# Kernel tuning notes

Hardware: AMD Instinct MI355X
Metric: run time of the kernel (lower is better)

Reference implementation:

```python
import jax, jax.numpy as jnp
import numpy as np

N_Q = 8
DIM = 2 ** N_Q          # 256
DEGREE = 3
ANSATZ_LAYERS = 2


def gelu(x):
    return jax.nn.gelu(x, approximate=False)


def layer_norm(x, g, b, eps=1e-5):
    mu = x.mean(-1, keepdims=True)
    v = x.var(-1, keepdims=True)
    return (x - mu) / jnp.sqrt(v + eps) * g + b


def apply_ry(state, theta, w, n):
    # state: (B, 2^n) complex64, theta: (B,) per-element angle
    half = theta * 0.5
    c, s = jnp.cos(half), jnp.sin(half)
    U = jnp.stack([jnp.stack([c, -s], -1), jnp.stack([s, c], -1)], -2).astype(state.dtype)
    L, R = 2 ** w, 2 ** (n - 1 - w)
    st = state.reshape(-1, L, 2, R)
    st = jnp.einsum('bij,bljr->blir', U, st)
    return st.reshape(state.shape)


def apply_crx(state, theta, c, t, n):
    # controlled-RX(theta), control wire c, target wire t (batched angles)
    half = theta * 0.5
    cs = jnp.cos(half).astype(state.dtype)
    ms = (-1j) * jnp.sin(half).astype(state.dtype)
    Rx = jnp.stack([jnp.stack([cs, ms], -1), jnp.stack([ms, cs], -1)], -2)  # (B,2,2)
    a, b = min(c, t), max(c, t)
    A, M, R = 2 ** a, 2 ** (b - a - 1), 2 ** (n - 1 - b)
    st = state.reshape(-1, A, 2, M, 2, R)
    if c < t:
        sub = st[:, :, 1]                              # control bit = 1 slice, (B,A,M,2,R)
        sub = jnp.einsum('bij,bamjr->bamir', Rx, sub)
        st = st.at[:, :, 1].set(sub)
    else:
        sub = st[:, :, :, :, 1]                        # (B,A,2,M,R)
        sub = jnp.einsum('bij,bajmr->baimr', Rx, sub)
        st = st.at[:, :, :, :, 1].set(sub)
    return st.reshape(state.shape)


def sim14(state, params, n, layers):
    # Sim et al. 2019 circuit 14: RY layer, CRX ring, RY layer, reversed CRX ring (4n params/layer)
    idx = 0
    for _ in range(layers):
        for q in range(n):
            state = apply_ry(state, params[:, idx + q], q, n)
        idx += n
        for q in range(n):
            state = apply_crx(state, params[:, idx + q], q, (q + 1) % n, n)
        idx += n
        for q in range(n):
            state = apply_ry(state, params[:, idx + q], q, n)
        idx += n
        for q in range(n):
            state = apply_crx(state, params[:, idx + q], q, (q - 1) % n, n)
        idx += n
    return state


def pauli_expvals(psi, n):
    # [<X_0..X_{n-1}>, <Y_0..>, <Z_0..>] for batched pure states psi: (B, 2^n)
    xs, ys, zs = [], [], []
    for w in range(n):
        L, R = 2 ** w, 2 ** (n - 1 - w)
        s = psi.reshape(-1, L, 2, R)
        s0, s1 = s[:, :, 0], s[:, :, 1]
        cross = (jnp.conj(s0) * s1).sum((1, 2))
        xs.append(2.0 * jnp.real(cross))
        ys.append(2.0 * jnp.imag(cross))
        zs.append((jnp.abs(s0) ** 2 - jnp.abs(s1) ** 2).sum((1, 2)))
    return jnp.stack(xs + ys + zs, axis=1).astype(jnp.float32)


def dwsep_conv(x, dw_w, dw_b, pw_w, pw_b, gn_g, gn_b, dilation):
    # depthwise-separable conv1d + GroupNorm(8) + GELU; x: (B, C, T)
    k = dw_w.shape[-1]
    pad = (k - 1) * dilation // 2
    y = jax.lax.conv_general_dilated(
        x, dw_w, window_strides=(1,), padding=[(pad, pad)], rhs_dilation=(dilation,),
        feature_group_count=x.shape[1], dimension_numbers=('NCH', 'OIH', 'NCH'))
    y = y + dw_b[None, :, None]
    y = jnp.einsum('oc,bct->bot', pw_w, y) + pw_b[None, :, None]
    B, C, T = y.shape
    g = y.reshape(B, 8, C // 8, T)
    mu = g.mean((2, 3), keepdims=True)
    var = g.var((2, 3), keepdims=True)
    y = ((g - mu) / jnp.sqrt(var + 1e-5)).reshape(B, C, T)
    return gelu(y * gn_g[None, :, None] + gn_b[None, :, None])


def setup_inputs() -> dict:
    key = jax.random.key(0)
    ks = iter(jax.random.split(key, 64))
    rn = lambda *s: jax.random.normal(next(ks), s, jnp.float32) * 0.05
    ru = lambda *s: jax.random.uniform(next(ks), s, dtype=jnp.float32)
    inp = dict(
        x=jax.random.normal(next(ks), (16, 363, 180), jnp.float32),
        net_w=rn(12, 15, 8), net_b=rn(12, 8),
        dwa_w=rn(96, 1, 7), dwa_b=rn(96), pwa_w=rn(96, 96), pwa_b=rn(96),
        gna_g=jnp.ones(96, jnp.float32), gna_b=jnp.zeros(96, jnp.float32),
        dwb_w=rn(96, 1, 7), dwb_b=rn(96), pwb_w=rn(96, 96), pwb_b=rn(96),
        gnb_g=jnp.ones(96, jnp.float32), gnb_b=jnp.zeros(96, jnp.float32),
        dwc_w=rn(96, 1, 7), dwc_b=rn(96), pwc_w=rn(96, 96), pwc_b=rn(96),
        gnc_g=jnp.ones(96, jnp.float32), gnc_b=jnp.zeros(96, jnp.float32),
        merge_w=rn(288, 128), merge_b=rn(128),
        merge_ln_g=jnp.ones(128, jnp.float32), merge_ln_b=jnp.zeros(128, jnp.float32),
        qproj_w=rn(128, 64), qproj_b=rn(64),
        poly_coeffs=ru(4), qff_params=ru(32),
        mix_re=ru(363), mix_im=ru(363),
        qout_w=rn(24, 128), qout_b=rn(128),
        fc_w=rn(78, 64), fc_b=rn(64),
        fus1_w=rn(192, 128), fus1_b=rn(128),
        fus_ln_g=jnp.ones(128, jnp.float32), fus_ln_b=jnp.zeros(128, jnp.float32),
        fus2_w=rn(128, 64), fus2_b=rn(64),
    )
    return inp


def reference(x, net_w, net_b, dwa_w, dwa_b, pwa_w, pwa_b, gna_g, gna_b,
              dwb_w, dwb_b, pwb_w, pwb_b, gnb_g, gnb_b,
              dwc_w, dwc_b, pwc_w, pwc_b, gnc_g, gnc_b,
              merge_w, merge_b, merge_ln_g, merge_ln_b,
              qproj_w, qproj_b, poly_coeffs, qff_params, mix_re, mix_im,
              qout_w, qout_b, fc_w, fc_b,
              fus1_w, fus1_b, fus_ln_g, fus_ln_b, fus2_w, fus2_b):
    B, T, C = x.shape
    # --- network projection: 12 contiguous networks of 15 ROIs -> d_net=8 each ---
    h = jnp.einsum('btki,kid->btkd', x.reshape(B, T, 12, 15), net_w) + net_b
    h = gelu(h).reshape(B, T, 96)
    # --- multiscale depthwise-separable convs ---
    ht = h.transpose(0, 2, 1)  # (B,96,T)
    a = dwsep_conv(ht, dwa_w, dwa_b, pwa_w, pwa_b, gna_g, gna_b, 1)
    b = dwsep_conv(ht, dwb_w, dwb_b, pwb_w, pwb_b, gnb_g, gnb_b, 4)
    c = dwsep_conv(ht, dwc_w, dwc_b, pwc_w, pwc_b, gnc_g, gnc_b, 16)
    cat = jnp.concatenate([a, b, c], axis=1).transpose(0, 2, 1)  # (B,T,288)
    h = gelu(layer_norm(cat @ merge_w + merge_b, merge_ln_g, merge_ln_b))  # (B,T,128)
    # --- QSVT quantum temporal mixing ---
    tp = jax.nn.sigmoid(h @ qproj_w + qproj_b) * (2.0 * np.pi)  # (B,T,64) rotation angles
    tp = tp.reshape(B * T, -1)
    base = jnp.zeros((B * T, DIM), jnp.complex64).at[:, 0].set(1.0)
    pc = poly_coeffs.astype(jnp.complex64)
    state = base
    acc = pc[0] * base
    for d in range(1, DEGREE + 1):
        state = sim14(state, tp, N_Q, ANSATZ_LAYERS)
        acc = acc + pc[d] * state
    acc = acc.reshape(B, T, DIM)
    mix = (mix_re + 1j * mix_im).astype(jnp.complex64)[:T]
    mixed = jnp.einsum('t,btd->bd', mix, acc)           # temporal mixing
    norm = jnp.linalg.norm(mixed, axis=1, keepdims=True)
    psi = mixed / (norm + 1e-9)
    psi = sim14(psi, jnp.broadcast_to(qff_params[None, :], (B, qff_params.shape[0])), N_Q, 1)
    exps = pauli_expvals(psi, N_Q)                      # (B,24)
    temporal = exps @ qout_w + qout_b                   # (B,128)
    # --- FC fingerprint ---
    xm = x - x.mean(1, keepdims=True)
    std = jnp.maximum(jnp.std(x, axis=1, keepdims=True, ddof=1), 1e-8)
    xn = xm / std
    corr = jnp.einsum('btc,btd->bcd', xn, xn) / (T - 1)
    bm = corr.reshape(B, 12, 15, 12, 15).mean((2, 4))   # (B,12,12) network-block means
    iu0, iu1 = jnp.triu_indices(12)
    fc_vec = bm[:, iu0, iu1]                            # (B,78)
    fc = gelu(fc_vec @ fc_w + fc_b)                     # (B,64)
    # --- fusion ---
    fused = jnp.concatenate([temporal, fc], axis=1)
    out = gelu(layer_norm(fused @ fus1_w + fus1_b, fus_ln_g, fus_ln_b)) @ fus2_w + fus2_b
    return out  # (B,64)
```

## Files before the change

### kernel.cpp

```cpp
#include <hip/hip_runtime.h>
#include <math.h>

#define NB 16
#define NT 363
#define NC 180
#define SZF 557568
#define NROW 5808

__device__ __forceinline__ float gelu_f(float x) {
  return 0.5f * x * (1.0f + erff(x * 0.7071067811865475244f));
}


template<int CTRL>
__device__ __forceinline__ float dppf(float x) {
  return __int_as_float(__builtin_amdgcn_update_dpp(
      0, __float_as_int(x), CTRL, 0xF, 0xF, true));
}

template<int LB>
__device__ __forceinline__ float lx(float x) {
  if constexpr (LB == 0) return dppf<0xB1>(x);
  else if constexpr (LB == 1) return dppf<0x4E>(x);
  else if constexpr (LB == 2) return __shfl_xor(x, 4);
  else return __shfl_xor(x, 8);
}

template<int P>
__device__ __forceinline__ void ry_local(float* re, float* im, float c, float s) {
#pragma unroll
  for (int j = 0; j < 16; ++j) {
    if ((j & (1 << P)) == 0) {
      int k = j | (1 << P);
      float r0 = re[j], i0 = im[j], r1 = re[k], i1 = im[k];
      re[j] = fmaf(c, r0, -s * r1); im[j] = fmaf(c, i0, -s * i1);
      re[k] = fmaf(s, r0,  c * r1); im[k] = fmaf(s, i0,  c * i1);
    }
  }
}

template<int LB>
__device__ __forceinline__ void ry_lane(float* re, float* im, float c, float s, int lane) {
  float sg = (lane & (1 << LB)) ? s : -s;
#pragma unroll
  for (int j = 0; j < 16; ++j) {
    float br = lx<LB>(re[j]);
    float bi = lx<LB>(im[j]);
    re[j] = fmaf(c, re[j], sg * br);
    im[j] = fmaf(c, im[j], sg * bi);
  }
}

template<int Q, int P>
__device__ __forceinline__ void crx_ll(float* re, float* im, float cs, float sn) {
#pragma unroll
  for (int j = 0; j < 16; ++j) {
    if ((j & (1 << Q)) && !(j & (1 << P))) {
      int k = j | (1 << P);
      float r0 = re[j], i0 = im[j], r1 = re[k], i1 = im[k];
      re[j] = fmaf(cs, r0,  sn * i1); im[j] = fmaf(cs, i0, -sn * r1);
      re[k] = fmaf(cs, r1,  sn * i0); im[k] = fmaf(cs, i1, -sn * r0);
    }
  }
}

template<int LBQ, int P>
__device__ __forceinline__ void crx_nl(float* re, float* im, float cs, float sn, int lane) {
  if (lane & (1 << LBQ)) {
#pragma unroll
    for (int j = 0; j < 16; ++j) {
      if ((j & (1 << P)) == 0) {
        int k = j | (1 << P);
        float r0 = re[j], i0 = im[j], r1 = re[k], i1 = im[k];
        re[j] = fmaf(cs, r0,  sn * i1); im[j] = fmaf(cs, i0, -sn * r1);
        re[k] = fmaf(cs, r1,  sn * i0); im[k] = fmaf(cs, i1, -sn * r0);
      }
    }
  }
}

template<int Q, int LBP>
__device__ __forceinline__ void crx_ln(float* re, float* im, float cs, float sn) {
#pragma unroll
  for (int j = 0; j < 16; ++j) {
    if (j & (1 << Q)) {
      float br = lx<LBP>(re[j]);
      float bi = lx<LBP>(im[j]);
      re[j] = fmaf(cs, re[j],  sn * bi);
      im[j] = fmaf(cs, im[j], -sn * br);
    }
  }
}

template<int LBQ, int LBP>
__device__ __forceinline__ void crx_nn(float* re, float* im, float cs, float sn, int lane) {
  bool ctl = (lane & (1 << LBQ)) != 0;
#pragma unroll
  for (int j = 0; j < 16; ++j) {
    float br = lx<LBP>(re[j]);
    float bi = lx<LBP>(im[j]);
    if (ctl) {
      re[j] = fmaf(cs, re[j],  sn * bi);
      im[j] = fmaf(cs, im[j], -sn * br);
    }
  }
}

__device__ __forceinline__ void qlayer(float* re, float* im,
                                       const float2* ang, int lane) {
  float2 a;
  a = ang[0];  ry_lane<3>(re, im, a.x, a.y, lane);
  a = ang[1];  ry_lane<2>(re, im, a.x, a.y, lane);
  a = ang[2];  ry_lane<1>(re, im, a.x, a.y, lane);
  a = ang[3];  ry_lane<0>(re, im, a.x, a.y, lane);
  a = ang[4];  ry_local<3>(re, im, a.x, a.y);
  a = ang[5];  ry_local<2>(re, im, a.x, a.y);
  a = ang[6];  ry_local<1>(re, im, a.x, a.y);
  a = ang[7];  ry_local<0>(re, im, a.x, a.y);
  a = ang[8];  crx_nn<3, 2>(re, im, a.x, a.y, lane);
  a = ang[9];  crx_nn<2, 1>(re, im, a.x, a.y, lane);
  a = ang[10]; crx_nn<1, 0>(re, im, a.x, a.y, lane);
  a = ang[11]; crx_nl<0, 3>(re, im, a.x, a.y, lane);
  a = ang[12]; crx_ll<3, 2>(re, im, a.x, a.y);
  a = ang[13]; crx_ll<2, 1>(re, im, a.x, a.y);
  a = ang[14]; crx_ll<1, 0>(re, im, a.x, a.y);
  a = ang[15]; crx_ln<0, 3>(re, im, a.x, a.y);
  a = ang[16]; ry_lane<3>(re, im, a.x, a.y, lane);
  a = ang[17]; ry_lane<2>(re, im, a.x, a.y, lane);
  a = ang[18]; ry_lane<1>(re, im, a.x, a.y, lane);
  a = ang[19]; ry_lane<0>(re, im, a.x, a.y, lane);
  a = ang[20]; ry_local<3>(re, im, a.x, a.y);
  a = ang[21]; ry_local<2>(re, im, a.x, a.y);
  a = ang[22]; ry_local<1>(re, im, a.x, a.y);
  a = ang[23]; ry_local<0>(re, im, a.x, a.y);
  a = ang[24]; crx_nl<3, 0>(re, im, a.x, a.y, lane);
  a = ang[25]; crx_nn<2, 3>(re, im, a.x, a.y, lane);
  a = ang[26]; crx_nn<1, 2>(re, im, a.x, a.y, lane);
  a = ang[27]; crx_nn<0, 1>(re, im, a.x, a.y, lane);
  a = ang[28]; crx_ln<3, 0>(re, im, a.x, a.y);
  a = ang[29]; crx_ll<2, 3>(re, im, a.x, a.y);
  a = ang[30]; crx_ll<1, 2>(re, im, a.x, a.y);
  a = ang[31]; crx_ll<0, 1>(re, im, a.x, a.y);
}

template<int P>
__device__ __forceinline__ void ryg(float* re, float* im, float c, float s, int lane) {
  if constexpr (P >= 2) {
    constexpr int mask = 1 << (P - 2);
    float sg = ((lane >> (P - 2)) & 1) ? s : -s;
#pragma unroll
    for (int j = 0; j < 4; ++j) {
      float br = __shfl_xor(re[j], mask);
      float bi = __shfl_xor(im[j], mask);
      re[j] = fmaf(c, re[j], sg * br);
      im[j] = fmaf(c, im[j], sg * bi);
    }
  } else {
#pragma unroll
    for (int k = 0; k < 2; ++k) {
      const int a = (P == 0) ? 2 * k : k;
      const int b = (P == 0) ? a + 1 : a + 2;
      float r0 = re[a], i0 = im[a], r1 = re[b], i1 = im[b];
      re[a] = fmaf(c, r0, -s * r1); im[a] = fmaf(c, i0, -s * i1);
      re[b] = fmaf(s, r0,  c * r1); im[b] = fmaf(s, i0,  c * i1);
    }
  }
}

template<int PC, int PT>
__device__ __forceinline__ void crxg(float* re, float* im, float cs, float sn, int lane) {
  if constexpr (PT >= 2) {
    constexpr int mask = 1 << (PT - 2);
#pragma unroll
    for (int j = 0; j < 4; ++j) {
      float br = __shfl_xor(re[j], mask);
      float bi = __shfl_xor(im[j], mask);
      bool ctrl;
      if constexpr (PC >= 2) ctrl = ((lane >> (PC - 2)) & 1) != 0;
      else                   ctrl = ((j >> PC) & 1) != 0;
      if (ctrl) {
        float nr = fmaf(cs, re[j],  sn * bi);
        float ni = fmaf(cs, im[j], -sn * br);
        re[j] = nr; im[j] = ni;
      }
    }
  } else {
#pragma unroll
    for (int k = 0; k < 2; ++k) {
      const int a = (PT == 0) ? 2 * k : k;
      const int b = (PT == 0) ? a + 1 : a + 2;
      bool ctrl;
      if constexpr (PC >= 2) ctrl = ((lane >> (PC - 2)) & 1) != 0;
      else                   ctrl = ((a >> PC) & 1) != 0;
      if (ctrl) {
        float r0 = re[a], i0 = im[a], r1 = re[b], i1 = im[b];
        re[a] = fmaf(cs, r0,  sn * i1); im[a] = fmaf(cs, i0, -sn * r1);
        re[b] = fmaf(cs, r1,  sn * i0); im[b] = fmaf(cs, i1, -sn * r0);
      }
    }
  }
}

__device__ __forceinline__ void sim14_layer(float* re, float* im,
                                            const float* Cr, const float* Sr, int lane) {
#define ARY1(q, pi) ryg<7-(q)>(re, im, Cr[pi], Sr[pi], lane)
#define ACX1(cq, tq, pi) crxg<7-(cq), 7-(tq)>(re, im, Cr[pi], Sr[pi], lane)
  ARY1(0,0); ARY1(1,1); ARY1(2,2); ARY1(3,3); ARY1(4,4); ARY1(5,5); ARY1(6,6); ARY1(7,7);
  ACX1(0,1,8); ACX1(1,2,9); ACX1(2,3,10); ACX1(3,4,11); ACX1(4,5,12); ACX1(5,6,13); ACX1(6,7,14); ACX1(7,0,15);
  ARY1(0,16); ARY1(1,17); ARY1(2,18); ARY1(3,19); ARY1(4,20); ARY1(5,21); ARY1(6,22); ARY1(7,23);
  ACX1(0,7,24); ACX1(1,0,25); ACX1(2,1,26); ACX1(3,2,27); ACX1(4,3,28); ACX1(5,4,29); ACX1(6,5,30); ACX1(7,6,31);
#undef ARY1
#undef ACX1
}

struct CorrSM { float mu[180]; float inv[180]; float S[NT * 12]; float fcv[78]; };
struct EmdwSM {
  float xs[NT * 15];
  float nwL[120], nbL[8];
  float hrow[8][368];
  float wL[3][8][8];
  float bL[3][8];
};
union EDSM { EmdwSM e; CorrSM c; };

__global__ __launch_bounds__(256) void k_emdw(const float* __restrict__ x,
    const float* __restrict__ nw, const float* __restrict__ nb,
    const float* __restrict__ wa, const float* __restrict__ ba,
    const float* __restrict__ wb, const float* __restrict__ bb,
    const float* __restrict__ wc, const float* __restrict__ bc,
    float* __restrict__ y1base,
    const float* __restrict__ fcw, const float* __restrict__ fcb,
    float* __restrict__ fusedG) {
  __shared__ EDSM sm;
  int b = blockIdx.x, kg = blockIdx.y, tid = threadIdx.x;
  if (kg < 12) {
    for (int i = tid; i < 120; i += 256) sm.e.nwL[i] = nw[kg * 120 + i];
    for (int i = tid; i < 8; i += 256) sm.e.nbL[i] = nb[kg * 8 + i];
    for (int i = tid; i < 168; i += 256) {
      int z = i / 56, r = i % 56, d = r / 7, k = r % 7;
      const float* w = (z == 0) ? wa : ((z == 1) ? wb : wc);
      sm.e.wL[z][d][k] = w[(kg * 8 + d) * 7 + k];
    }
    for (int i = tid; i < 24; i += 256) {
      int z = i / 8, d = i % 8;
      const float* bias = (z == 0) ? ba : ((z == 1) ? bb : bc);
      sm.e.bL[z][d] = bias[kg * 8 + d];
    }
    for (int i = tid; i < NT * 15; i += 256) {
      int t = i / 15, u = i % 15;
      sm.e.xs[i] = x[((size_t)b * NT + t) * NC + kg * 15 + u];
    }
    __syncthreads();
    for (int i = tid; i < 8 * NT; i += 256) {
      int t = i % NT, d = i / NT;
      float acc2 = sm.e.nbL[d];
#pragma unroll
      for (int u = 0; u < 15; ++u) acc2 = fmaf(sm.e.xs[t * 15 + u], sm.e.nwL[u * 8 + d], acc2);
      sm.e.hrow[d][t] = gelu_f(acc2);
    }
    __syncthreads();
    for (int i = tid; i < 8 * NT; i += 256) {
      int t = i % NT, d = i / NT;
      int c = kg * 8 + d;
      float a0 = sm.e.bL[0][d], a1 = sm.e.bL[1][d], a2 = sm.e.bL[2][d];
#pragma unroll
      for (int k = 0; k < 7; ++k) {
        int i1 = t + (k - 3);
        int i4 = t + (k - 3) * 4;
        int i16 = t + (k - 3) * 16;
        if (i1 >= 0 && i1 < NT)  a0 = fmaf(sm.e.hrow[d][i1],  sm.e.wL[0][d][k], a0);
        if (i4 >= 0 && i4 < NT)  a1 = fmaf(sm.e.hrow[d][i4],  sm.e.wL[1][d][k], a1);
        if (i16 >= 0 && i16 < NT) a2 = fmaf(sm.e.hrow[d][i16], sm.e.wL[2][d][k], a2);
      }
      size_t base = ((size_t)b * 96 + c) * NT + t;
      y1base[base] = a0;
      y1base[SZF + base] = a1;
      y1base[2 * SZF + base] = a2;
    }
  } else {
    if (tid < 180) {
      float s = 0;
      const float* px = x + (size_t)b * NT * NC + tid;
      for (int t = 0; t < NT; ++t) s += px[t * NC];
      float mu = s / 363.0f;
      float q = 0;
      for (int t = 0; t < NT; ++t) { float d = px[t * NC] - mu; q = fmaf(d, d, q); }
      float sd = sqrtf(q / 362.0f);
      sd = fmaxf(sd, 1e-8f);
      sm.c.mu[tid] = mu; sm.c.inv[tid] = 1.0f / sd;
    }
    __syncthreads();
    for (int t = tid; t < NT; t += 256) {
      const float* px = x + (size_t)(b * NT + t) * NC;
#pragma unroll
      for (int i = 0; i < 12; ++i) {
        float s = 0;
#pragma unroll
        for (int u = 0; u < 15; ++u) {
          int cidx = i * 15 + u;
          s += (px[cidx] - sm.c.mu[cidx]) * sm.c.inv[cidx];
        }
        sm.c.S[t * 12 + i] = s;
      }
    }
    __syncthreads();
    if (tid < 78) {
      int i = 0, rem = tid;
      while (rem >= 12 - i) { rem -= 12 - i; ++i; }
      int j = i + rem;
      float acc = 0;
      for (int t = 0; t < NT; ++t) acc = fmaf(sm.c.S[t * 12 + i], sm.c.S[t * 12 + j], acc);
      sm.c.fcv[tid] = acc * (1.0f / (225.0f * 362.0f));
    }
    __syncthreads();
    if (tid < 64) {
      float v = fcb[tid];
#pragma unroll
      for (int k = 0; k < 78; ++k) v = fmaf(sm.c.fcv[k], fcw[k * 64 + tid], v);
      fusedG[b * 192 + 128 + tid] = gelu_f(v);
    }
  }
}

__global__ __launch_bounds__(256) void k_pw(const float* __restrict__ y1base,
    const float* __restrict__ wA, const float* __restrict__ wB, const float* __restrict__ wC,
    const float* __restrict__ bA, const float* __restrict__ bB, const float* __restrict__ bC,
    float* __restrict__ y2base) {
  int b = blockIdx.x, tile = blockIdx.y, z = blockIdx.z, tid = threadIdx.x;
  const float* pw_w = (z == 0) ? wA : ((z == 1) ? wB : wC);
  const float* pw_b = (z == 0) ? bA : ((z == 1) ? bB : bC);
  const float* y1 = y1base + (size_t)z * SZF;
  float* y2 = y2base + (size_t)z * SZF;
  int t0 = tile * 64;
  __shared__ float y1t[96 * 64];
  __shared__ float pwL[96 * 97];
  for (int i = tid; i < 96 * 96; i += 256) {
    int o = i / 96, cc = i % 96;
    pwL[o * 97 + cc] = pw_w[i];
  }
  for (int i = tid; i < 96 * 64; i += 256) {
    int cc = i >> 6, t = i & 63;
    int tt = t0 + t;
    y1t[i] = (tt < NT) ? y1[(b * 96 + cc) * NT + tt] : 0.0f;
  }
  __syncthreads();
  int o16 = tid >> 4, t4 = (tid & 15) * 4;
  for (int pass = 0; pass < 6; ++pass) {
    int o = pass * 16 + o16;
    float bias = pw_b[o];
    float a0 = bias, a1 = bias, a2 = bias, a3 = bias;
    const float* wrow = &pwL[o * 97];
#pragma unroll 4
    for (int cc = 0; cc < 96; ++cc) {
      const float4 vy = *reinterpret_cast<const float4*>(&y1t[cc * 64 + t4]);
      float w = wrow[cc];
      a0 = fmaf(w, vy.x, a0); a1 = fmaf(w, vy.y, a1);
      a2 = fmaf(w, vy.z, a2); a3 = fmaf(w, vy.w, a3);
    }
    int base = (b * 96 + o) * NT;
    int t = t0 + t4;
    if (t + 3 < NT) {
      y2[base + t] = a0; y2[base + t + 1] = a1; y2[base + t + 2] = a2; y2[base + t + 3] = a3;
    } else {
      if (t < NT) y2[base + t] = a0;
      if (t + 1 < NT) y2[base + t + 1] = a1;
      if (t + 2 < NT) y2[base + t + 2] = a2;
      if (t + 3 < NT) y2[base + t + 3] = a3;
    }
  }
}

__global__ __launch_bounds__(256) void k_gn(const float* __restrict__ y2base,
    const float* __restrict__ gA, const float* __restrict__ gB, const float* __restrict__ gC,
    const float* __restrict__ bA, const float* __restrict__ bB, const float* __restrict__ bC,
    float* __restrict__ cat) {
  int b = blockIdx.x, tile = blockIdx.y, z = blockIdx.z, tid = threadIdx.x;
  const float* gng = (z == 0) ? gA : ((z == 1) ? gB : gC);
  const float* gnb = (z == 0) ? bA : ((z == 1) ? bB : bC);
  const float* y2 = y2base + (size_t)z * SZF + (size_t)b * 96 * NT;
  __shared__ float redS[256], redQ[256];
  __shared__ float muL[8], rsL[8];
  __shared__ float yL[96 * 65];
  for (int g = 0; g < 8; ++g) {
    const float* gb = y2 + g * 12 * NT;
    float s = 0, q = 0;
    for (int i = tid; i < 12 * NT; i += 256) { float v = gb[i]; s += v; q = fmaf(v, v, q); }
    redS[tid] = s; redQ[tid] = q;
    __syncthreads();
    for (int st = 128; st > 0; st >>= 1) {
      if (tid < st) { redS[tid] += redS[tid + st]; redQ[tid] += redQ[tid + st]; }
      __syncthreads();
    }
    if (tid == 0) {
      float mu = redS[0] / 4356.0f;
      float var = redQ[0] / 4356.0f - mu * mu;
      muL[g] = mu;
      rsL[g] = rsqrtf(fmaxf(var, 0.0f) + 1e-5f);
    }
    __syncthreads();
  }
  int t0 = tile * 64;
  for (int i = tid; i < 96 * 64; i += 256) {
    int cc = i >> 6, t = i & 63;
    int tt = t0 + t;
    yL[cc * 65 + t] = (tt < NT) ? y2[cc * NT + tt] : 0.0f;
  }
  __syncthreads();
  for (int i = tid; i < 64 * 96; i += 256) {
    int tt = i / 96, cc = i % 96;
    int t = t0 + tt;
    if (t < NT) {
      int g = cc / 12;
      float v = (yL[cc * 65 + tt] - muL[g]) * rsL[g] * gng[cc] + gnb[cc];
      cat[((size_t)b * NT + t) * 288 + z * 96 + cc] = gelu_f(v);
    }
  }
}

__global__ __launch_bounds__(256) void k_merge(const float* __restrict__ cat,
    const float* __restrict__ mw, const float* __restrict__ mb,
    const float* __restrict__ lng, const float* __restrict__ lnb,
    const float* __restrict__ qw, const float* __restrict__ qb,
    float2* __restrict__ angG) {
  int blk = blockIdx.x, tid = threadIdx.x;
  __shared__ float catL[8][288];
  __shared__ float vL[8][129];
  __shared__ float hL[8][129];
  __shared__ float muS[8], rsS[8];
  for (int i = tid; i < 8 * 288; i += 256) {
    int r = i / 288, k = i % 288;
    catL[r][k] = cat[((size_t)blk * 8 + r) * 288 + k];
  }
  __syncthreads();
  int jj = tid & 127, rg = tid >> 7;
  float bias = mb[jj];
  float acc[4] = {bias, bias, bias, bias};
  for (int k = 0; k < 288; ++k) {
    float w = mw[k * 128 + jj];
#pragma unroll
    for (int r = 0; r < 4; ++r) acc[r] = fmaf(catL[rg * 4 + r][k], w, acc[r]);
  }
#pragma unroll
  for (int r = 0; r < 4; ++r) vL[rg * 4 + r][jj] = acc[r];
  __syncthreads();
  if (tid < 8) {
    float s = 0;
    for (int k = 0; k < 128; ++k) s += vL[tid][k];
    float mu = s / 128.0f;
    float q = 0;
    for (int k = 0; k < 128; ++k) { float d = vL[tid][k] - mu; q = fmaf(d, d, q); }
    muS[tid] = mu;
    rsS[tid] = rsqrtf(q / 128.0f + 1e-5f);
  }
  __syncthreads();
  float g = lng[jj], bb2 = lnb[jj];
#pragma unroll
  for (int r = 0; r < 4; ++r) {
    int row = rg * 4 + r;
    float h = (acc[r] - muS[row]) * rsS[row] * g + bb2;
    hL[row][jj] = gelu_f(h);
  }
  __syncthreads();
  int o = tid & 63;
  int r0 = (tid >> 6) * 2;
  for (int rr = 0; rr < 2; ++rr) {
    int row = r0 + rr;
    float u = qb[o];
    for (int k = 0; k < 128; ++k) u = fmaf(hL[row][k], qw[k * 64 + o], u);
    float tp = 6.2831853071795864769f / (1.0f + expf(-u));
    float hf = tp * 0.5f;
    int grow = blk * 8 + row;
    angG[(size_t)grow * 64 + o] = make_float2(cosf(hf), sinf(hf));
  }
}

__global__ __launch_bounds__(64) void k_quantum(const float2* __restrict__ angG,
                                                const float* __restrict__ pc4,
                                                float* __restrict__ accG) {
  const int lane = threadIdx.x;
  const int g = lane >> 4;
  const int ll = lane & 15;
  const int row0 = blockIdx.x * 4;
  __shared__ float2 angL[4][66];
#pragma unroll
  for (int q = 0; q < 4; ++q)
    angL[q][lane] = angG[(size_t)(row0 + q) * 64 + lane];
  __syncthreads();
  float p0 = pc4[0], p1 = pc4[1], p2 = pc4[2], p3 = pc4[3];
  float re[16], im[16];
#pragma unroll
  for (int j = 0; j < 16; ++j) { re[j] = 0.0f; im[j] = 0.0f; }
  if (ll == 0) re[0] = p3;
  const float2* ang = &angL[g][0];
  for (int rep = 0; rep < 3; ++rep) {
    qlayer(re, im, ang, lane);
    qlayer(re, im, ang + 32, lane);
    float pc = (rep == 0) ? p2 : (rep == 1) ? p1 : p0;
    if (ll == 0) re[0] += pc;
  }
  int row = row0 + g;
  float4* dst = reinterpret_cast<float4*>(accG + ((size_t)row * 256 + ll * 16) * 2);
#pragma unroll
  for (int h = 0; h < 8; ++h)
    dst[h] = make_float4(re[2 * h], im[2 * h], re[2 * h + 1], im[2 * h + 1]);
}

__global__ __launch_bounds__(256) void k_tail(const float* __restrict__ accG,
    const float* __restrict__ mr, const float* __restrict__ mi,
    const float* __restrict__ qff,
    const float* __restrict__ qout_w, const float* __restrict__ qout_b,
    const float* __restrict__ fusedG,
    const float* __restrict__ w1, const float* __restrict__ b1,
    const float* __restrict__ lng, const float* __restrict__ lnb,
    const float* __restrict__ w2, const float* __restrict__ b2,
    float* __restrict__ out) {
  int b = blockIdx.x, tid = threadIdx.x;
  __shared__ float psiL[256][2];
  __shared__ float red[256];
  __shared__ float qcL[32], qsL[32], exps[24];
  __shared__ float tL[128], cL[64], hL[128];
  {
    const float2* av = reinterpret_cast<const float2*>(accG) + (size_t)b * NT * 256 + tid;
    float sr0 = 0, si0 = 0, sr1 = 0, si1 = 0;
#pragma unroll 4
    for (int t = 0; t < NT - 1; t += 2) {
      float2 a0 = av[(size_t)t * 256];
      float2 a1 = av[(size_t)(t + 1) * 256];
      float m0r = mr[t], m0i = mi[t];
      float m1r = mr[t + 1], m1i = mi[t + 1];
      sr0 = fmaf(m0r, a0.x, fmaf(-m0i, a0.y, sr0));
      si0 = fmaf(m0r, a0.y, fmaf(m0i, a0.x, si0));
      sr1 = fmaf(m1r, a1.x, fmaf(-m1i, a1.y, sr1));
      si1 = fmaf(m1r, a1.y, fmaf(m1i, a1.x, si1));
    }
    {
      float2 a = av[(size_t)(NT - 1) * 256];
      float m_r = mr[NT - 1], m_i = mi[NT - 1];
      sr0 = fmaf(m_r, a.x, fmaf(-m_i, a.y, sr0));
      si0 = fmaf(m_r, a.y, fmaf(m_i, a.x, si0));
    }
    float sr = sr0 + sr1, si = si0 + si1;
    psiL[tid][0] = sr; psiL[tid][1] = si;
    red[tid] = sr * sr + si * si;
  }
  if (tid < 32) { float h = qff[tid] * 0.5f; qcL[tid] = cosf(h); qsL[tid] = sinf(h); }
  __syncthreads();
  for (int s2 = 128; s2 > 0; s2 >>= 1) { if (tid < s2) red[tid] += red[tid + s2]; __syncthreads(); }
  float inv = 1.0f / (sqrtf(red[0]) + 1e-9f);
  __syncthreads();
  if (tid < 64) {
    int lane = tid;
    float re[4], im[4];
#pragma unroll
    for (int j = 0; j < 4; ++j) {
      re[j] = psiL[lane * 4 + j][0] * inv;
      im[j] = psiL[lane * 4 + j][1] * inv;
    }
    sim14_layer(re, im, qcL, qsL, lane);
#pragma unroll
    for (int j = 0; j < 4; ++j) { psiL[lane * 4 + j][0] = re[j]; psiL[lane * 4 + j][1] = im[j]; }
  }
  __syncthreads();
  if (tid < 64) {
    int lane = tid;
    for (int w = 0; w < 8; ++w) {
      int p = 7 - w;
      float cr = 0, ci = 0, z = 0;
#pragma unroll
      for (int k = 0; k < 2; ++k) {
        int pr = lane + k * 64;
        int lowmask = (1 << p) - 1;
        int i0 = ((pr >> p) << (p + 1)) | (pr & lowmask);
        int i1 = i0 | (1 << p);
        float r0 = psiL[i0][0], I0 = psiL[i0][1], r1 = psiL[i1][0], I1 = psiL[i1][1];
        cr += r0 * r1 + I0 * I1;
        ci += r0 * I1 - I0 * r1;
        z += r0 * r0 + I0 * I0 - r1 * r1 - I1 * I1;
      }
      for (int off = 32; off > 0; off >>= 1) {
        cr += __shfl_down(cr, off);
        ci += __shfl_down(ci, off);
        z  += __shfl_down(z, off);
      }
      if (lane == 0) { exps[w] = 2.0f * cr; exps[8 + w] = 2.0f * ci; exps[16 + w] = z; }
    }
  }
  __syncthreads();
  if (tid < 128) {
    float v = qout_b[tid];
#pragma unroll
    for (int k = 0; k < 24; ++k) v = fmaf(exps[k], qout_w[k * 128 + tid], v);
    tL[tid] = v;
  } else if (tid < 192) {
    cL[tid - 128] = fusedG[b * 192 + 128 + (tid - 128)];
  }
  __syncthreads();
  float v = 0.0f;
  if (tid < 128) {
    v = b1[tid];
    for (int k = 0; k < 128; ++k) v = fmaf(tL[k], w1[k * 128 + tid], v);
    for (int k = 0; k < 64; ++k)  v = fmaf(cL[k], w1[(128 + k) * 128 + tid], v);
    red[tid] = v;
  }
  __syncthreads();
  for (int s = 64; s > 0; s >>= 1) { if (tid < s) red[tid] += red[tid + s]; __syncthreads(); }
  float mu = red[0] / 128.0f;
  __syncthreads();
  float dv = v - mu;
  if (tid < 128) red[tid] = dv * dv;
  __syncthreads();
  for (int s = 64; s > 0; s >>= 1) { if (tid < s) red[tid] += red[tid + s]; __syncthreads(); }
  float var = red[0] / 128.0f;
  if (tid < 128) hL[tid] = gelu_f(dv * rsqrtf(var + 1e-5f) * lng[tid] + lnb[tid]);
  __syncthreads();
  if (tid < 64) {
    float o = b2[tid];
    for (int k = 0; k < 128; ++k) o = fmaf(hL[k], w2[k * 64 + tid], o);
    out[b * 64 + tid] = o;
  }
}

extern "C" void kernel_launch(void* const* d_in, const int* in_sizes, int n_in,
                              void* d_out, int out_size, void* d_ws, size_t ws_size,
                              hipStream_t stream) {
  const float* x       = (const float*)d_in[0];
  const float* net_w   = (const float*)d_in[1];
  const float* net_b   = (const float*)d_in[2];
  const float* dwa_w   = (const float*)d_in[3];
  const float* dwa_b   = (const float*)d_in[4];
  const float* pwa_w   = (const float*)d_in[5];
  const float* pwa_b   = (const float*)d_in[6];
  const float* gna_g   = (const float*)d_in[7];
  const float* gna_b   = (const float*)d_in[8];
  const float* dwb_w   = (const float*)d_in[9];
  const float* dwb_b   = (const float*)d_in[10];
  const float* pwb_w   = (const float*)d_in[11];
  const float* pwb_b   = (const float*)d_in[12];
  const float* gnb_g   = (const float*)d_in[13];
  const float* gnb_b   = (const float*)d_in[14];
  const float* dwc_w   = (const float*)d_in[15];
  const float* dwc_b   = (const float*)d_in[16];
  const float* pwc_w   = (const float*)d_in[17];
  const float* pwc_b   = (const float*)d_in[18];
  const float* gnc_g   = (const float*)d_in[19];
  const float* gnc_b   = (const float*)d_in[20];
  const float* merge_w = (const float*)d_in[21];
  const float* merge_b = (const float*)d_in[22];
  const float* mlng    = (const float*)d_in[23];
  const float* mlnb    = (const float*)d_in[24];
  const float* qproj_w = (const float*)d_in[25];
  const float* qproj_b = (const float*)d_in[26];
  const float* poly    = (const float*)d_in[27];
  const float* qff     = (const float*)d_in[28];
  const float* mix_re  = (const float*)d_in[29];
  const float* mix_im  = (const float*)d_in[30];
  const float* qout_w  = (const float*)d_in[31];
  const float* qout_b  = (const float*)d_in[32];
  const float* fc_w    = (const float*)d_in[33];
  const float* fc_b    = (const float*)d_in[34];
  const float* fus1_w  = (const float*)d_in[35];
  const float* fus1_b  = (const float*)d_in[36];
  const float* flng    = (const float*)d_in[37];
  const float* flnb    = (const float*)d_in[38];
  const float* fus2_w  = (const float*)d_in[39];
  const float* fus2_b  = (const float*)d_in[40];
  float* out = (float*)d_out;

  float* W = (float*)d_ws;
  float* y1b_  = W;
  float* cat   = W;
  float* y2b_  = W + 3 * (size_t)SZF;
  float* acc   = W;
  float2* angG = (float2*)(W + 6 * (size_t)SZF);
  float* fused = W + 6 * (size_t)SZF + 743424;

  k_emdw<<<dim3(NB, 13), 256, 0, stream>>>(x, net_w, net_b,
      dwa_w, dwa_b, dwb_w, dwb_b, dwc_w, dwc_b, y1b_, fc_w, fc_b, fused);
  k_pw<<<dim3(NB, 6, 3), 256, 0, stream>>>(y1b_, pwa_w, pwb_w, pwc_w, pwa_b, pwb_b, pwc_b, y2b_);
  k_gn<<<dim3(NB, 6, 3), 256, 0, stream>>>(y2b_,
      gna_g, gnb_g, gnc_g, gna_b, gnb_b, gnc_b, cat);
  k_merge<<<726, 256, 0, stream>>>(cat, merge_w, merge_b, mlng, mlnb,
      qproj_w, qproj_b, angG);
  k_quantum<<<NROW / 4, 64, 0, stream>>>(angG, poly, acc);
  k_tail<<<NB, 256, 0, stream>>>(acc, mix_re, mix_im, qff, qout_w, qout_b, fused,
                                 fus1_w, fus1_b, flng, flnb, fus2_w, fus2_b, out);
}
```

Measured before the change: 365.4 us.

## Split group-norm statistics and temporal mixing into separate parallel kernels

```diff
diff --git a/kernel.cpp b/kernel.cpp
--- a/kernel.cpp
+++ b/kernel.cpp
@@ -370,40 +370,46 @@
   }
 }
 
-__global__ __launch_bounds__(256) void k_gn(const float* __restrict__ y2base,
+__global__ __launch_bounds__(256) void k_gnstat(const float* __restrict__ y2base,
+                                                float* __restrict__ muG,
+                                                float* __restrict__ rsG) {
+  int b = blockIdx.x, g = blockIdx.y, z = blockIdx.z, tid = threadIdx.x;
+  __shared__ float red[256];
+  const float* base = y2base + (size_t)z * SZF + (b * 96 + g * 12) * NT;
+  float s = 0;
+  for (int i = tid; i < 12 * NT; i += 256) s += base[i];
+  red[tid] = s; __syncthreads();
+  for (int st = 128; st > 0; st >>= 1) { if (tid < st) red[tid] += red[tid + st]; __syncthreads(); }
+  float mu = red[0] / 4356.0f;
+  __syncthreads();
+  float q = 0;
+  for (int i = tid; i < 12 * NT; i += 256) { float d = base[i] - mu; q = fmaf(d, d, q); }
+  red[tid] = q; __syncthreads();
+  for (int st = 128; st > 0; st >>= 1) { if (tid < st) red[tid] += red[tid + st]; __syncthreads(); }
+  if (tid == 0) {
+    float var = red[0] / 4356.0f;
+    muG[(z * NB + b) * 8 + g] = mu;
+    rsG[(z * NB + b) * 8 + g] = rsqrtf(var + 1e-5f);
+  }
+}
+
+__global__ __launch_bounds__(256) void k_gnapply(const float* __restrict__ y2base,
+    const float* __restrict__ muG, const float* __restrict__ rsG,
     const float* __restrict__ gA, const float* __restrict__ gB, const float* __restrict__ gC,
     const float* __restrict__ bA, const float* __restrict__ bB, const float* __restrict__ bC,
     float* __restrict__ cat) {
   int b = blockIdx.x, tile = blockIdx.y, z = blockIdx.z, tid = threadIdx.x;
   const float* gng = (z == 0) ? gA : ((z == 1) ? gB : gC);
   const float* gnb = (z == 0) ? bA : ((z == 1) ? bB : bC);
-  const float* y2 = y2base + (size_t)z * SZF + (size_t)b * 96 * NT;
-  __shared__ float redS[256], redQ[256];
+  const float* y2 = y2base + (size_t)z * SZF;
+  int t0 = tile * 64;
+  __shared__ float yL[96 * 65];
   __shared__ float muL[8], rsL[8];
-  __shared__ float yL[96 * 65];
-  for (int g = 0; g < 8; ++g) {
-    const float* gb = y2 + g * 12 * NT;
-    float s = 0, q = 0;
-    for (int i = tid; i < 12 * NT; i += 256) { float v = gb[i]; s += v; q = fmaf(v, v, q); }
-    redS[tid] = s; redQ[tid] = q;
-    __syncthreads();
-    for (int st = 128; st > 0; st >>= 1) {
-      if (tid < st) { redS[tid] += redS[tid + st]; redQ[tid] += redQ[tid + st]; }
-      __syncthreads();
-    }
-    if (tid == 0) {
-      float mu = redS[0] / 4356.0f;
-      float var = redQ[0] / 4356.0f - mu * mu;
-      muL[g] = mu;
-      rsL[g] = rsqrtf(fmaxf(var, 0.0f) + 1e-5f);
-    }
-    __syncthreads();
-  }
-  int t0 = tile * 64;
+  if (tid < 8) { muL[tid] = muG[(z * NB + b) * 8 + tid]; rsL[tid] = rsG[(z * NB + b) * 8 + tid]; }
   for (int i = tid; i < 96 * 64; i += 256) {
     int cc = i >> 6, t = i & 63;
     int tt = t0 + t;
-    yL[cc * 65 + t] = (tt < NT) ? y2[cc * NT + tt] : 0.0f;
+    yL[cc * 65 + t] = (tt < NT) ? y2[(b * 96 + cc) * NT + tt] : 0.0f;
   }
   __syncthreads();
   for (int i = tid; i < 64 * 96; i += 256) {
@@ -505,8 +511,25 @@
     dst[h] = make_float4(re[2 * h], im[2 * h], re[2 * h + 1], im[2 * h + 1]);
 }
 
-__global__ __launch_bounds__(256) void k_tail(const float* __restrict__ accG,
-    const float* __restrict__ mr, const float* __restrict__ mi,
+__global__ __launch_bounds__(256) void k_mix1(const float* __restrict__ accG,
+                                              const float* __restrict__ mr,
+                                              const float* __restrict__ mi,
+                                              float* __restrict__ part) {
+  int b = blockIdx.x, ch = blockIdx.y, d = threadIdx.x;
+  int t0 = ch * 33;
+  float sr = 0, si = 0;
+  for (int i = 0; i < 33; ++i) {
+    int t = t0 + i;
+    const float2 a = *reinterpret_cast<const float2*>(accG + (size_t)((b * NT + t) * 256 + d) * 2);
+    float m_r = mr[t], m_i = mi[t];
+    sr = fmaf(m_r, a.x, fmaf(-m_i, a.y, sr));
+    si = fmaf(m_r, a.y, fmaf(m_i, a.x, si));
+  }
+  float2* o = reinterpret_cast<float2*>(part + (size_t)((b * 11 + ch) * 256 + d) * 2);
+  *o = make_float2(sr, si);
+}
+
+__global__ __launch_bounds__(256) void k_tail(const float* __restrict__ part,
     const float* __restrict__ qff,
     const float* __restrict__ qout_w, const float* __restrict__ qout_b,
     const float* __restrict__ fusedG,
@@ -520,26 +543,11 @@
   __shared__ float qcL[32], qsL[32], exps[24];
   __shared__ float tL[128], cL[64], hL[128];
   {
-    const float2* av = reinterpret_cast<const float2*>(accG) + (size_t)b * NT * 256 + tid;
-    float sr0 = 0, si0 = 0, sr1 = 0, si1 = 0;
-#pragma unroll 4
-    for (int t = 0; t < NT - 1; t += 2) {
-      float2 a0 = av[(size_t)t * 256];
-      float2 a1 = av[(size_t)(t + 1) * 256];
-      float m0r = mr[t], m0i = mi[t];
-      float m1r = mr[t + 1], m1i = mi[t + 1];
-      sr0 = fmaf(m0r, a0.x, fmaf(-m0i, a0.y, sr0));
-      si0 = fmaf(m0r, a0.y, fmaf(m0i, a0.x, si0));
-      sr1 = fmaf(m1r, a1.x, fmaf(-m1i, a1.y, sr1));
-      si1 = fmaf(m1r, a1.y, fmaf(m1i, a1.x, si1));
-    }
-    {
-      float2 a = av[(size_t)(NT - 1) * 256];
-      float m_r = mr[NT - 1], m_i = mi[NT - 1];
-      sr0 = fmaf(m_r, a.x, fmaf(-m_i, a.y, sr0));
-      si0 = fmaf(m_r, a.y, fmaf(m_i, a.x, si0));
-    }
-    float sr = sr0 + sr1, si = si0 + si1;
+    float sr = 0, si = 0;
+    for (int ch = 0; ch < 11; ++ch) {
+      const float2 a = *reinterpret_cast<const float2*>(part + (size_t)((b * 11 + ch) * 256 + tid) * 2);
+      sr += a.x; si += a.y;
+    }
     psiL[tid][0] = sr; psiL[tid][1] = si;
     red[tid] = sr * sr + si * si;
   }
@@ -672,16 +680,21 @@
   float* y2b_  = W + 3 * (size_t)SZF;
   float* acc   = W;
   float2* angG = (float2*)(W + 6 * (size_t)SZF);
-  float* fused = W + 6 * (size_t)SZF + 743424;
+  float* muG   = W + 6 * (size_t)SZF + 743424;
+  float* rsG   = muG + 512;
+  float* part  = rsG + 512;
+  float* fused = part + 90112;
 
   k_emdw<<<dim3(NB, 13), 256, 0, stream>>>(x, net_w, net_b,
       dwa_w, dwa_b, dwb_w, dwb_b, dwc_w, dwc_b, y1b_, fc_w, fc_b, fused);
   k_pw<<<dim3(NB, 6, 3), 256, 0, stream>>>(y1b_, pwa_w, pwb_w, pwc_w, pwa_b, pwb_b, pwc_b, y2b_);
-  k_gn<<<dim3(NB, 6, 3), 256, 0, stream>>>(y2b_,
+  k_gnstat<<<dim3(NB, 8, 3), 256, 0, stream>>>(y2b_, muG, rsG);
+  k_gnapply<<<dim3(NB, 6, 3), 256, 0, stream>>>(y2b_, muG, rsG,
       gna_g, gnb_g, gnc_g, gna_b, gnb_b, gnc_b, cat);
   k_merge<<<726, 256, 0, stream>>>(cat, merge_w, merge_b, mlng, mlnb,
       qproj_w, qproj_b, angG);
   k_quantum<<<NROW / 4, 64, 0, stream>>>(angG, poly, acc);
-  k_tail<<<NB, 256, 0, stream>>>(acc, mix_re, mix_im, qff, qout_w, qout_b, fused,
+  k_mix1<<<dim3(NB, 11), 256, 0, stream>>>(acc, mix_re, mix_im, part);
+  k_tail<<<NB, 256, 0, stream>>>(part, qff, qout_w, qout_b, fused,
                                  fus1_w, fus1_b, flng, flnb, fus2_w, fus2_b, out);
 }
```

New measurement: 316.8 us (median of 2 runs). 1.15x faster.
